# Performance work log

Measured on AMD Instinct MI355X. Metric: run time of the kernel, lower is better.

## Reference

```python
import jax, jax.numpy as jnp
import numpy as np

B, N, E = 16, 1024, 32768
D_IN, HID, HEADS, OUT = 33, 32, 4, 8  # OUT = d_mid // heads
EPS = 1e-5
NEG_SLOPE = 0.2  # PyG GATConv default leaky_relu slope


def layer_norm(x, g, b):
    m = x.mean(-1, keepdims=True)
    v = ((x - m) ** 2).mean(-1, keepdims=True)
    return (x - m) / jnp.sqrt(v + EPS) * g + b


def gat_conv(x, src, dst, W, a_src, a_dst, bias):
    # x: [N, F_in]; W: [F_in, HEADS*OUT]; a_src/a_dst: [HEADS, OUT]
    n = x.shape[0]
    xp = (x @ W).reshape(n, HEADS, OUT)                 # [N, H, D]
    al_s = (xp * a_src).sum(-1)                          # [N, H]
    al_d = (xp * a_dst).sum(-1)                          # [N, H]
    e = jax.nn.leaky_relu(al_s[src] + al_d[dst], NEG_SLOPE)  # [E, H]
    # softmax over incoming edges per target node (PyG: softmax over edge_index[1])
    m = jax.ops.segment_max(e, dst, num_segments=n)
    ex = jnp.exp(e - m[dst])
    s = jax.ops.segment_sum(ex, dst, num_segments=n)
    alpha = ex / s[dst]                                  # [E, H]
    out = jax.ops.segment_sum(xp[src] * alpha[:, :, None], dst, num_segments=n)
    return out.reshape(n, HEADS * OUT) + bias, alpha


def setup_inputs() -> dict:
    key = jax.random.key(0)
    ks = jax.random.split(key, 16)
    inp = {
        "H": jax.random.normal(ks[0], (B, N, D_IN), jnp.float32),
        "edge_index": jax.random.randint(ks[1], (2, E), 0, N, dtype=jnp.int64),
        # ObsEmbedding params
        "W1_e": jax.random.normal(ks[2], (D_IN, HID), jnp.float32) * 0.1,
        "b1_e": jnp.zeros((HID,), jnp.float32),
        "W2_e": jax.random.normal(ks[3], (HID, HID), jnp.float32) * 0.1,
        "b2_e": jnp.zeros((HID,), jnp.float32),
        "ln_e_g": jnp.ones((HID,), jnp.float32),
        "ln_e_b": jnp.zeros((HID,), jnp.float32),
        # GAT1 params
        "W_g1": jax.random.normal(ks[4], (HID, HEADS * OUT), jnp.float32) * 0.1,
        "as_g1": jax.random.normal(ks[5], (HEADS, OUT), jnp.float32) * 0.1,
        "ad_g1": jax.random.normal(ks[6], (HEADS, OUT), jnp.float32) * 0.1,
        "bi_g1": jnp.zeros((HEADS * OUT,), jnp.float32),
        # GAT2 params
        "W_g2": jax.random.normal(ks[7], (HEADS * OUT, HEADS * OUT), jnp.float32) * 0.1,
        "as_g2": jax.random.normal(ks[8], (HEADS, OUT), jnp.float32) * 0.1,
        "ad_g2": jax.random.normal(ks[9], (HEADS, OUT), jnp.float32) * 0.1,
        "bi_g2": jnp.zeros((HEADS * OUT,), jnp.float32),
        # output LayerNorm
        "ln_o_g": jnp.ones((HEADS * OUT,), jnp.float32),
        "ln_o_b": jnp.zeros((HEADS * OUT,), jnp.float32),
    }
    return inp


def reference(H, edge_index, W1_e, b1_e, W2_e, b2_e, ln_e_g, ln_e_b,
              W_g1, as_g1, ad_g1, bi_g1, W_g2, as_g2, ad_g2, bi_g2,
              ln_o_g, ln_o_b):
    src, dst = edge_index[0], edge_index[1]

    # ObsEmbedding: Linear->ReLU->Linear->ReLU->LayerNorm (batched, dense)
    x = jax.nn.relu(H @ W1_e + b1_e)
    x = jax.nn.relu(x @ W2_e + b2_e)
    x = layer_norm(x, ln_e_g, ln_e_b)          # [B, N, 32]

    def per_graph(xb):
        h1, _ = gat_conv(xb, src, dst, W_g1, as_g1, ad_g1, bi_g1)
        h1 = jax.nn.relu(h1)
        h2, alpha2 = gat_conv(h1, src, dst, W_g2, as_g2, ad_g2, bi_g2)
        h_out = layer_norm(h1 + h2, ln_o_g, ln_o_b)
        return h_out, alpha2

    h_out, alpha2 = jax.vmap(per_graph)(x)      # [B, N, 32], [B, E, HEADS]

    # scatter edge attention into dense [B, HEADS, N, N] at [src, dst]
    alpha_t = jnp.transpose(alpha2, (0, 2, 1))  # [B, HEADS, E]
    A = jnp.zeros((B, HEADS, N, N), jnp.float32).at[:, :, src, dst].set(alpha_t)
    return h_out, A
```

## Files before the change

kernel.cpp:

```cpp
#include <hip/hip_runtime.h>
#include <hip/hip_bf16.h>

#define BB 16
#define NN 1024
#define EE 32768
#define D_IN 33
#define HID 32
#define HEADS 4
#define OUTD 8
#define FF 32
#define EPSL 1e-5f
#define SLOPE 0.2f

__device__ __forceinline__ float red32(float v) {
    v += __shfl_xor(v, 1);
    v += __shfl_xor(v, 2);
    v += __shfl_xor(v, 4);
    v += __shfl_xor(v, 8);
    v += __shfl_xor(v, 16);
    return v;
}
__device__ __forceinline__ float red8(float v) {
    v += __shfl_xor(v, 1);
    v += __shfl_xor(v, 2);
    v += __shfl_xor(v, 4);
    return v;
}
__device__ __forceinline__ void wb() { __builtin_amdgcn_wave_barrier(); }

struct EmbedS {
    float sW1[D_IN * 32];
    float sW2[1024];
    float sWg[1024];
    float sb1[32], sb2[32], sg[32], sbt[32], sas[32], sad[32];
    float sh[8][34];
    float sx[8][33];
};
struct CsrS {
    int hh[1024];
    int hh2[1024];
    int sp[256];
};

__global__ __launch_bounds__(256) void k_embed_csr(
    const float* __restrict__ Hm, const float* __restrict__ W1,
    const float* __restrict__ b1, const float* __restrict__ W2,
    const float* __restrict__ b2, const float* __restrict__ lng,
    const float* __restrict__ lnb, const float* __restrict__ Wg1,
    const float* __restrict__ as1, const float* __restrict__ ad1,
    float* __restrict__ xp1, float* __restrict__ als1, float* __restrict__ ald1,
    const int* __restrict__ ei, int* __restrict__ off, int* __restrict__ cur,
    int* __restrict__ off2, int* __restrict__ cur2) {
    __shared__ union { EmbedS e; CsrS c; } sm;
    int tid = threadIdx.x;
    if (blockIdx.x == 2048) {
        int t = tid;
#pragma unroll
        for (int i = 0; i < 4; i++) { sm.c.hh[t + 256 * i] = 0; sm.c.hh2[t + 256 * i] = 0; }
        __syncthreads();
        for (int e = t; e < EE; e += 256) {
            int s = ei[e], d = ei[EE + e];
            atomicAdd(&sm.c.hh[d], 1);
            atomicAdd(&sm.c.hh2[s], 1);
        }
        __syncthreads();
        {
            int a0 = sm.c.hh[4 * t], a1 = sm.c.hh[4 * t + 1];
            int a2 = sm.c.hh[4 * t + 2], a3 = sm.c.hh[4 * t + 3];
            int s0 = a0, s01 = a0 + a1, s012 = s01 + a2, tot = s012 + a3;
            sm.c.sp[t] = tot;
            __syncthreads();
            for (int st = 1; st < 256; st <<= 1) {
                int u = (t >= st) ? sm.c.sp[t - st] : 0;
                __syncthreads();
                sm.c.sp[t] += u;
                __syncthreads();
            }
            int ex = t ? sm.c.sp[t - 1] : 0;
            off[4 * t + 1] = ex + s0; off[4 * t + 2] = ex + s01;
            off[4 * t + 3] = ex + s012; off[4 * t + 4] = ex + tot;
            if (t == 0) off[0] = 0;
            cur[4 * t] = ex; cur[4 * t + 1] = ex + s0;
            cur[4 * t + 2] = ex + s01; cur[4 * t + 3] = ex + s012;
            __syncthreads();
        }
        {
            int a0 = sm.c.hh2[4 * t], a1 = sm.c.hh2[4 * t + 1];
            int a2 = sm.c.hh2[4 * t + 2], a3 = sm.c.hh2[4 * t + 3];
            int s0 = a0, s01 = a0 + a1, s012 = s01 + a2, tot = s012 + a3;
            sm.c.sp[t] = tot;
            __syncthreads();
            for (int st = 1; st < 256; st <<= 1) {
                int u = (t >= st) ? sm.c.sp[t - st] : 0;
                __syncthreads();
                sm.c.sp[t] += u;
                __syncthreads();
            }
            int ex = t ? sm.c.sp[t - 1] : 0;
            off2[4 * t + 1] = ex + s0; off2[4 * t + 2] = ex + s01;
            off2[4 * t + 3] = ex + s012; off2[4 * t + 4] = ex + tot;
            if (t == 0) off2[0] = 0;
            cur2[4 * t] = ex; cur2[4 * t + 1] = ex + s0;
            cur2[4 * t + 2] = ex + s01; cur2[4 * t + 3] = ex + s012;
        }
        return;
    }
    for (int i = tid; i < D_IN * 32; i += 256) sm.e.sW1[i] = W1[i];
    for (int i = tid; i < 1024; i += 256) { sm.e.sW2[i] = W2[i]; sm.e.sWg[i] = Wg1[i]; }
    if (tid < 32) {
        sm.e.sb1[tid] = b1[tid]; sm.e.sb2[tid] = b2[tid];
        sm.e.sg[tid] = lng[tid]; sm.e.sbt[tid] = lnb[tid];
        sm.e.sas[tid] = as1[tid]; sm.e.sad[tid] = ad1[tid];
    }
    int g = tid >> 5, j = tid & 31;
    int idx = blockIdx.x * 8 + g;
    __syncthreads();
    int base = idx * D_IN;
    for (int i = j; i < D_IN; i += 32) sm.e.sh[g][i] = Hm[base + i];
    wb();
    float acc = sm.e.sb1[j];
#pragma unroll
    for (int i = 0; i < D_IN; i++) acc += sm.e.sh[g][i] * sm.e.sW1[i * 32 + j];
    float x1 = fmaxf(acc, 0.f);
    sm.e.sx[g][j] = x1;
    wb();
    acc = sm.e.sb2[j];
#pragma unroll
    for (int i = 0; i < 32; i++) acc += sm.e.sx[g][i] * sm.e.sW2[i * 32 + j];
    float x2 = fmaxf(acc, 0.f);
    float mean = red32(x2) * (1.f / 32.f);
    float d0 = x2 - mean;
    float var = red32(d0 * d0) * (1.f / 32.f);
    float xn = d0 * rsqrtf(var + EPSL) * sm.e.sg[j] + sm.e.sbt[j];
    wb();
    sm.e.sx[g][j] = xn;
    wb();
    acc = 0.f;
#pragma unroll
    for (int i = 0; i < 32; i++) acc += sm.e.sx[g][i] * sm.e.sWg[i * 32 + j];
    xp1[idx * 32 + j] = acc;
    float ps = red8(acc * sm.e.sas[j]);
    float pd = red8(acc * sm.e.sad[j]);
    if ((j & 7) == 0) {
        als1[idx * 4 + (j >> 3)] = ps;
        ald1[idx * 4 + (j >> 3)] = pd;
    }
}

__global__ __launch_bounds__(256) void k_fill(const int* __restrict__ ei,
                                              int* __restrict__ cur,
                                              int* __restrict__ csr_src,
                                              int* __restrict__ cur2,
                                              int* __restrict__ out_dst) {
    int e = blockIdx.x * 256 + threadIdx.x;
    if (e < EE) {
        int s = ei[e], d = ei[EE + e];
        int p = atomicAdd(&cur[d], 1);
        csr_src[p] = s;
        int p2 = atomicAdd(&cur2[s], 1);
        out_dst[p2] = d;
    }
}

__global__ __launch_bounds__(256) void k_gat1(
    const int* __restrict__ off, const int* __restrict__ csr_src,
    const float* __restrict__ xp1, const float* __restrict__ als1,
    const float* __restrict__ ald1, const float* __restrict__ bi1,
    const float* __restrict__ Wg2, const float* __restrict__ as2,
    const float* __restrict__ ad2, float* __restrict__ h1,
    float* __restrict__ xp2, float* __restrict__ als2, float* __restrict__ ald2) {
    __shared__ float sW[1024];
    __shared__ float sb[32], sas[32], sad[32];
    __shared__ float sx[8][33];
    __shared__ float salp[8][32];
    __shared__ int   ssrc[8][8];
    int tid = threadIdx.x;
    for (int i = tid; i < 1024; i += 256) sW[i] = Wg2[i];
    if (tid < 32) { sb[tid] = bi1[tid]; sas[tid] = as2[tid]; sad[tid] = ad2[tid]; }
    __syncthreads();
    int g = tid >> 5, j = tid & 31, h = j >> 3, t8 = j & 7;
    int idx = blockIdx.x * 8 + g;
    int b = idx >> 10, n = idx & 1023;
    int beg = off[n], end = off[n + 1];
    float aldh = ald1[idx * 4 + h];
    const float* alsb = als1 + b * NN * 4;
    const float* xpb = xp1 + b * NN * 32;
    float se = 0.f, acc = 0.f;
    for (int kb = beg; kb < end; kb += 8) {
        int k = kb + t8;
        float al = 0.f; int s = 0;
        if (k < end) {
            s = csr_src[k];
            float av = alsb[s * 4 + h] + aldh;
            av = av > 0.f ? av : SLOPE * av;
            al = __expf(av);
        }
        se += al;
        salp[g][j] = al;
        if (h == 0) ssrc[g][t8] = s;
        wb();
#pragma unroll
        for (int t = 0; t < 8; t++)
            acc += salp[g][(h << 3) + t] * xpb[ssrc[g][t] * 32 + j];
        wb();
    }
    se = red8(se);
    float inv = se > 0.f ? 1.f / se : 0.f;
    acc *= inv;
    float hv = fmaxf(acc + sb[j], 0.f);
    h1[idx * 32 + j] = hv;
    sx[g][j] = hv;
    wb();
    float x2 = 0.f;
#pragma unroll
    for (int i = 0; i < 32; i++) x2 += sx[g][i] * sW[i * 32 + j];
    xp2[idx * 32 + j] = x2;
    float ps = red8(x2 * sas[j]);
    float pd = red8(x2 * sad[j]);
    if (t8 == 0) {
        als2[idx * 4 + h] = ps;
        ald2[((b * 4 + h) << 10) + n] = pd;
    }
}

__global__ __launch_bounds__(256) void k_gat2(
    const int* __restrict__ off, const int* __restrict__ csr_src,
    const float* __restrict__ xp2, const float* __restrict__ als2,
    const float* __restrict__ ald2, const float* __restrict__ h1,
    const float* __restrict__ bi2, const float* __restrict__ lng,
    const float* __restrict__ lnb, float* __restrict__ outH,
    float* __restrict__ dinv) {
    __shared__ float sb[32], sg[32], sbt[32];
    __shared__ float salp[8][32];
    __shared__ int   ssrc[8][8];
    int tid = threadIdx.x;
    if (tid < 32) { sb[tid] = bi2[tid]; sg[tid] = lng[tid]; sbt[tid] = lnb[tid]; }
    __syncthreads();
    int g = tid >> 5, j = tid & 31, h = j >> 3, t8 = j & 7;
    int idx = blockIdx.x * 8 + g;
    int b = idx >> 10, n = idx & 1023;
    int beg = off[n], end = off[n + 1];
    float aldh = ald2[((b * 4 + h) << 10) + n];
    const float* alsb = als2 + b * NN * 4;
    const float* xpb = xp2 + b * NN * 32;
    float se = 0.f, acc = 0.f;
    for (int kb = beg; kb < end; kb += 8) {
        int k = kb + t8;
        float al = 0.f; int s = 0;
        if (k < end) {
            s = csr_src[k];
            float av = alsb[s * 4 + h] + aldh;
            av = av > 0.f ? av : SLOPE * av;
            al = __expf(av);
        }
        se += al;
        salp[g][j] = al;
        if (h == 0) ssrc[g][t8] = s;
        wb();
#pragma unroll
        for (int t = 0; t < 8; t++)
            acc += salp[g][(h << 3) + t] * xpb[ssrc[g][t] * 32 + j];
        wb();
    }
    se = red8(se);
    float inv = se > 0.f ? 1.f / se : 0.f;
    if (t8 == 0) dinv[((b * 4 + h) << 10) + n] = inv;
    acc *= inv;
    float y = h1[idx * 32 + j] + acc + sb[j];
    float mean = red32(y) * (1.f / 32.f);
    float d0 = y - mean;
    float var = red32(d0 * d0) * (1.f / 32.f);
    outH[idx * 32 + j] = d0 * rsqrtf(var + EPSL) * sg[j] + sbt[j];
}

#define ROWS_PER_BLOCK 4
__global__ __launch_bounds__(256) void k_rowA(
    const int* __restrict__ off2, const int* __restrict__ out_dst,
    const float* __restrict__ als2, const float* __restrict__ ald2,
    const float* __restrict__ dinv, float* __restrict__ A) {
    __shared__ float sRow[ROWS_PER_BLOCK][NN];
    int wid = threadIdx.x >> 6, lane = threadIdx.x & 63;
    int r = blockIdx.x * ROWS_PER_BLOCK + wid;
    int bh = r >> 10, src = r & 1023;
    int b = bh >> 2, h = bh & 3;
    float sS = als2[((b << 10) + src) * 4 + h];
    const float* aldv = ald2 + ((size_t)bh << 10);
    const float* dinvv = dinv + ((size_t)bh << 10);
    float4* row4 = (float4*)&sRow[wid][0];
    float4 z = make_float4(0.f, 0.f, 0.f, 0.f);
#pragma unroll
    for (int i = 0; i < 4; i++) row4[i * 64 + lane] = z;
    wb();
    int beg = off2[src], end = off2[src + 1];
    for (int p = beg + lane; p < end; p += 64) {
        int d = out_dst[p];
        float lg = sS + aldv[d];
        lg = lg > 0.f ? lg : SLOPE * lg;
        sRow[wid][d] = __expf(lg) * dinvv[d];
    }
    wb();
    float4* o4 = (float4*)(A + (size_t)bh * (NN * NN) + (size_t)src * NN);
#pragma unroll
    for (int i = 0; i < 4; i++) o4[i * 64 + lane] = row4[i * 64 + lane];
}

extern "C" void kernel_launch(void* const* d_in, const int* in_sizes, int n_in,
                              void* d_out, int out_size, void* d_ws, size_t ws_size,
                              hipStream_t stream) {
    const float* Hm  = (const float*)d_in[0];
    const int*   ei  = (const int*)d_in[1];
    const float* W1  = (const float*)d_in[2];
    const float* b1  = (const float*)d_in[3];
    const float* W2  = (const float*)d_in[4];
    const float* b2  = (const float*)d_in[5];
    const float* lneg = (const float*)d_in[6];
    const float* lneb = (const float*)d_in[7];
    const float* Wg1 = (const float*)d_in[8];
    const float* as1 = (const float*)d_in[9];
    const float* ad1 = (const float*)d_in[10];
    const float* bi1 = (const float*)d_in[11];
    const float* Wg2 = (const float*)d_in[12];
    const float* as2 = (const float*)d_in[13];
    const float* ad2 = (const float*)d_in[14];
    const float* bi2 = (const float*)d_in[15];
    const float* lnog = (const float*)d_in[16];
    const float* lnob = (const float*)d_in[17];

    float* outH = (float*)d_out;
    float* A    = outH + BB * NN * FF;

    int* off      = (int*)d_ws;
    int* cur      = off + 1028;
    int* off2     = cur + 1024;
    int* cur2     = off2 + 1028;
    int* csr_src  = cur2 + 1024;
    int* out_dst  = csr_src + EE;
    float* fb     = (float*)(out_dst + EE);
    float* xp1    = fb;
    float* als1   = xp1 + BB * NN * FF;
    float* ald1   = als1 + BB * NN * 4;
    float* h1     = ald1 + BB * NN * 4;
    float* xp2    = h1 + BB * NN * FF;
    float* als2   = xp2 + BB * NN * FF;
    float* ald2   = als2 + BB * NN * 4;
    float* dinv   = ald2 + BB * NN * 4;

    hipLaunchKernelGGL(k_embed_csr, dim3(BB * NN / 8 + 1), dim3(256), 0, stream,
                       Hm, W1, b1, W2, b2, lneg, lneb, Wg1, as1, ad1,
                       xp1, als1, ald1, ei, off, cur, off2, cur2);
    hipLaunchKernelGGL(k_fill, dim3(EE / 256), dim3(256), 0, stream,
                       ei, cur, csr_src, cur2, out_dst);
    hipLaunchKernelGGL(k_gat1, dim3(BB * NN / 8), dim3(256), 0, stream,
                       off, csr_src, xp1, als1, ald1, bi1, Wg2, as2, ad2,
                       h1, xp2, als2, ald2);
    hipLaunchKernelGGL(k_gat2, dim3(BB * NN / 8), dim3(256), 0, stream,
                       off, csr_src, xp2, als2, ald2, h1, bi2, lnog, lnob,
                       outH, dinv);
    hipLaunchKernelGGL(k_rowA, dim3(BB * HEADS * NN / ROWS_PER_BLOCK), dim3(256),
                       0, stream, off2, out_dst, als2, ald2, dinv, A);
}
```

Before: 417.6 us.

## Replace CSR build with fixed-capacity bucket adjacency and fuse into embed kernel

Replaces the single-block histogram plus prefix-scan CSR construction and the separate fill kernel with fixed-capacity per-node buckets (CAP=96). The buckets are filled by atomics in extra blocks of the embed kernel, after a memset of the counters. It also interleaves ald2 and dinv into one float2 array so the row-scatter kernel does one load per edge, and writes the dense A matrix with nontemporal stores. The serial scan block and one launch go away. The cost is that edge order within a bucket is now nondeterministic and any node with more than 96 edges would overflow its bucket.

Measured after the change: 347.4 us. 16.8% less time.

```diff
diff --git a/kernel.cpp b/kernel.cpp
--- a/kernel.cpp
+++ b/kernel.cpp
@@ -11,6 +11,9 @@
 #define FF 32
 #define EPSL 1e-5f
 #define SLOPE 0.2f
+#define CAP 96
+
+typedef float v4f __attribute__((ext_vector_type(4)));
 
 __device__ __forceinline__ float red32(float v) {
     v += __shfl_xor(v, 1);
@@ -28,147 +31,81 @@
 }
 __device__ __forceinline__ void wb() { __builtin_amdgcn_wave_barrier(); }
 
-struct EmbedS {
-    float sW1[D_IN * 32];
-    float sW2[1024];
-    float sWg[1024];
-    float sb1[32], sb2[32], sg[32], sbt[32], sas[32], sad[32];
-    float sh[8][34];
-    float sx[8][33];
-};
-struct CsrS {
-    int hh[1024];
-    int hh2[1024];
-    int sp[256];
-};
-
-__global__ __launch_bounds__(256) void k_embed_csr(
+__global__ __launch_bounds__(256) void k_embed_bucket(
     const float* __restrict__ Hm, const float* __restrict__ W1,
     const float* __restrict__ b1, const float* __restrict__ W2,
     const float* __restrict__ b2, const float* __restrict__ lng,
     const float* __restrict__ lnb, const float* __restrict__ Wg1,
     const float* __restrict__ as1, const float* __restrict__ ad1,
     float* __restrict__ xp1, float* __restrict__ als1, float* __restrict__ ald1,
-    const int* __restrict__ ei, int* __restrict__ off, int* __restrict__ cur,
-    int* __restrict__ off2, int* __restrict__ cur2) {
-    __shared__ union { EmbedS e; CsrS c; } sm;
+    const int* __restrict__ ei, int* __restrict__ cnt_in, int* __restrict__ cnt_out,
+    int* __restrict__ csr_b, int* __restrict__ out_b) {
     int tid = threadIdx.x;
-    if (blockIdx.x == 2048) {
-        int t = tid;
-#pragma unroll
-        for (int i = 0; i < 4; i++) { sm.c.hh[t + 256 * i] = 0; sm.c.hh2[t + 256 * i] = 0; }
-        __syncthreads();
-        for (int e = t; e < EE; e += 256) {
-            int s = ei[e], d = ei[EE + e];
-            atomicAdd(&sm.c.hh[d], 1);
-            atomicAdd(&sm.c.hh2[s], 1);
-        }
-        __syncthreads();
-        {
-            int a0 = sm.c.hh[4 * t], a1 = sm.c.hh[4 * t + 1];
-            int a2 = sm.c.hh[4 * t + 2], a3 = sm.c.hh[4 * t + 3];
-            int s0 = a0, s01 = a0 + a1, s012 = s01 + a2, tot = s012 + a3;
-            sm.c.sp[t] = tot;
-            __syncthreads();
-            for (int st = 1; st < 256; st <<= 1) {
-                int u = (t >= st) ? sm.c.sp[t - st] : 0;
-                __syncthreads();
-                sm.c.sp[t] += u;
-                __syncthreads();
-            }
-            int ex = t ? sm.c.sp[t - 1] : 0;
-            off[4 * t + 1] = ex + s0; off[4 * t + 2] = ex + s01;
-            off[4 * t + 3] = ex + s012; off[4 * t + 4] = ex + tot;
-            if (t == 0) off[0] = 0;
-            cur[4 * t] = ex; cur[4 * t + 1] = ex + s0;
-            cur[4 * t + 2] = ex + s01; cur[4 * t + 3] = ex + s012;
-            __syncthreads();
-        }
-        {
-            int a0 = sm.c.hh2[4 * t], a1 = sm.c.hh2[4 * t + 1];
-            int a2 = sm.c.hh2[4 * t + 2], a3 = sm.c.hh2[4 * t + 3];
-            int s0 = a0, s01 = a0 + a1, s012 = s01 + a2, tot = s012 + a3;
-            sm.c.sp[t] = tot;
-            __syncthreads();
-            for (int st = 1; st < 256; st <<= 1) {
-                int u = (t >= st) ? sm.c.sp[t - st] : 0;
-                __syncthreads();
-                sm.c.sp[t] += u;
-                __syncthreads();
-            }
-            int ex = t ? sm.c.sp[t - 1] : 0;
-            off2[4 * t + 1] = ex + s0; off2[4 * t + 2] = ex + s01;
-            off2[4 * t + 3] = ex + s012; off2[4 * t + 4] = ex + tot;
-            if (t == 0) off2[0] = 0;
-            cur2[4 * t] = ex; cur2[4 * t + 1] = ex + s0;
-            cur2[4 * t + 2] = ex + s01; cur2[4 * t + 3] = ex + s012;
-        }
+    if (blockIdx.x >= 2048) {
+        int e = (blockIdx.x - 2048) * 256 + tid;
+        int s = ei[e], d = ei[EE + e];
+        int p = atomicAdd(&cnt_in[d], 1);
+        csr_b[d * CAP + p] = s;
+        int q = atomicAdd(&cnt_out[s], 1);
+        out_b[s * CAP + q] = d;
         return;
     }
-    for (int i = tid; i < D_IN * 32; i += 256) sm.e.sW1[i] = W1[i];
-    for (int i = tid; i < 1024; i += 256) { sm.e.sW2[i] = W2[i]; sm.e.sWg[i] = Wg1[i]; }
+    __shared__ float sW1[D_IN * 32];
+    __shared__ float sW2[1024];
+    __shared__ float sWg[1024];
+    __shared__ float sb1[32], sb2[32], sg[32], sbt[32], sas[32], sad[32];
+    __shared__ float sh[8][34];
+    __shared__ float sx[8][33];
+    for (int i = tid; i < D_IN * 32; i += 256) sW1[i] = W1[i];
+    for (int i = tid; i < 1024; i += 256) { sW2[i] = W2[i]; sWg[i] = Wg1[i]; }
     if (tid < 32) {
-        sm.e.sb1[tid] = b1[tid]; sm.e.sb2[tid] = b2[tid];
-        sm.e.sg[tid] = lng[tid]; sm.e.sbt[tid] = lnb[tid];
-        sm.e.sas[tid] = as1[tid]; sm.e.sad[tid] = ad1[tid];
+        sb1[tid] = b1[tid]; sb2[tid] = b2[tid];
+        sg[tid] = lng[tid]; sbt[tid] = lnb[tid];
+        sas[tid] = as1[tid]; sad[tid] = ad1[tid];
     }
     int g = tid >> 5, j = tid & 31;
     int idx = blockIdx.x * 8 + g;
     __syncthreads();
     int base = idx * D_IN;
-    for (int i = j; i < D_IN; i += 32) sm.e.sh[g][i] = Hm[base + i];
-    wb();
-    float acc = sm.e.sb1[j];
-#pragma unroll
-    for (int i = 0; i < D_IN; i++) acc += sm.e.sh[g][i] * sm.e.sW1[i * 32 + j];
+    for (int i = j; i < D_IN; i += 32) sh[g][i] = Hm[base + i];
+    wb();
+    float acc = sb1[j];
+#pragma unroll
+    for (int i = 0; i < D_IN; i++) acc += sh[g][i] * sW1[i * 32 + j];
     float x1 = fmaxf(acc, 0.f);
-    sm.e.sx[g][j] = x1;
-    wb();
-    acc = sm.e.sb2[j];
-#pragma unroll
-    for (int i = 0; i < 32; i++) acc += sm.e.sx[g][i] * sm.e.sW2[i * 32 + j];
+    sx[g][j] = x1;
+    wb();
+    acc = sb2[j];
+#pragma unroll
+    for (int i = 0; i < 32; i++) acc += sx[g][i] * sW2[i * 32 + j];
     float x2 = fmaxf(acc, 0.f);
     float mean = red32(x2) * (1.f / 32.f);
     float d0 = x2 - mean;
     float var = red32(d0 * d0) * (1.f / 32.f);
-    float xn = d0 * rsqrtf(var + EPSL) * sm.e.sg[j] + sm.e.sbt[j];
-    wb();
-    sm.e.sx[g][j] = xn;
+    float xn = d0 * rsqrtf(var + EPSL) * sg[j] + sbt[j];
+    wb();
+    sx[g][j] = xn;
     wb();
     acc = 0.f;
 #pragma unroll
-    for (int i = 0; i < 32; i++) acc += sm.e.sx[g][i] * sm.e.sWg[i * 32 + j];
+    for (int i = 0; i < 32; i++) acc += sx[g][i] * sWg[i * 32 + j];
     xp1[idx * 32 + j] = acc;
-    float ps = red8(acc * sm.e.sas[j]);
-    float pd = red8(acc * sm.e.sad[j]);
+    float ps = red8(acc * sas[j]);
+    float pd = red8(acc * sad[j]);
     if ((j & 7) == 0) {
         als1[idx * 4 + (j >> 3)] = ps;
         ald1[idx * 4 + (j >> 3)] = pd;
     }
 }
 
-__global__ __launch_bounds__(256) void k_fill(const int* __restrict__ ei,
-                                              int* __restrict__ cur,
-                                              int* __restrict__ csr_src,
-                                              int* __restrict__ cur2,
-                                              int* __restrict__ out_dst) {
-    int e = blockIdx.x * 256 + threadIdx.x;
-    if (e < EE) {
-        int s = ei[e], d = ei[EE + e];
-        int p = atomicAdd(&cur[d], 1);
-        csr_src[p] = s;
-        int p2 = atomicAdd(&cur2[s], 1);
-        out_dst[p2] = d;
-    }
-}
-
 __global__ __launch_bounds__(256) void k_gat1(
-    const int* __restrict__ off, const int* __restrict__ csr_src,
+    const int* __restrict__ cnt_in, const int* __restrict__ csr_b,
     const float* __restrict__ xp1, const float* __restrict__ als1,
     const float* __restrict__ ald1, const float* __restrict__ bi1,
     const float* __restrict__ Wg2, const float* __restrict__ as2,
     const float* __restrict__ ad2, float* __restrict__ h1,
-    float* __restrict__ xp2, float* __restrict__ als2, float* __restrict__ ald2) {
+    float* __restrict__ xp2, float* __restrict__ als2,
+    float2* __restrict__ aldinv) {
     __shared__ float sW[1024];
     __shared__ float sb[32], sas[32], sad[32];
     __shared__ float sx[8][33];
@@ -181,16 +118,17 @@
     int g = tid >> 5, j = tid & 31, h = j >> 3, t8 = j & 7;
     int idx = blockIdx.x * 8 + g;
     int b = idx >> 10, n = idx & 1023;
-    int beg = off[n], end = off[n + 1];
+    int cnt = cnt_in[n];
+    const int* row = csr_b + n * CAP;
     float aldh = ald1[idx * 4 + h];
     const float* alsb = als1 + b * NN * 4;
     const float* xpb = xp1 + b * NN * 32;
     float se = 0.f, acc = 0.f;
-    for (int kb = beg; kb < end; kb += 8) {
+    for (int kb = 0; kb < cnt; kb += 8) {
         int k = kb + t8;
         float al = 0.f; int s = 0;
-        if (k < end) {
-            s = csr_src[k];
+        if (k < cnt) {
+            s = row[k];
             float av = alsb[s * 4 + h] + aldh;
             av = av > 0.f ? av : SLOPE * av;
             al = __expf(av);
@@ -219,17 +157,16 @@
     float pd = red8(x2 * sad[j]);
     if (t8 == 0) {
         als2[idx * 4 + h] = ps;
-        ald2[((b * 4 + h) << 10) + n] = pd;
+        aldinv[((b * 4 + h) << 10) + n].x = pd;
     }
 }
 
 __global__ __launch_bounds__(256) void k_gat2(
-    const int* __restrict__ off, const int* __restrict__ csr_src,
+    const int* __restrict__ cnt_in, const int* __restrict__ csr_b,
     const float* __restrict__ xp2, const float* __restrict__ als2,
-    const float* __restrict__ ald2, const float* __restrict__ h1,
+    float2* __restrict__ aldinv, const float* __restrict__ h1,
     const float* __restrict__ bi2, const float* __restrict__ lng,
-    const float* __restrict__ lnb, float* __restrict__ outH,
-    float* __restrict__ dinv) {
+    const float* __restrict__ lnb, float* __restrict__ outH) {
     __shared__ float sb[32], sg[32], sbt[32];
     __shared__ float salp[8][32];
     __shared__ int   ssrc[8][8];
@@ -239,16 +176,17 @@
     int g = tid >> 5, j = tid & 31, h = j >> 3, t8 = j & 7;
     int idx = blockIdx.x * 8 + g;
     int b = idx >> 10, n = idx & 1023;
-    int beg = off[n], end = off[n + 1];
-    float aldh = ald2[((b * 4 + h) << 10) + n];
+    int cnt = cnt_in[n];
+    const int* row = csr_b + n * CAP;
+    float aldh = aldinv[((b * 4 + h) << 10) + n].x;
     const float* alsb = als2 + b * NN * 4;
     const float* xpb = xp2 + b * NN * 32;
     float se = 0.f, acc = 0.f;
-    for (int kb = beg; kb < end; kb += 8) {
+    for (int kb = 0; kb < cnt; kb += 8) {
         int k = kb + t8;
         float al = 0.f; int s = 0;
-        if (k < end) {
-            s = csr_src[k];
+        if (k < cnt) {
+            s = row[k];
             float av = alsb[s * 4 + h] + aldh;
             av = av > 0.f ? av : SLOPE * av;
             al = __expf(av);
@@ -264,7 +202,7 @@
     }
     se = red8(se);
     float inv = se > 0.f ? 1.f / se : 0.f;
-    if (t8 == 0) dinv[((b * 4 + h) << 10) + n] = inv;
+    if (t8 == 0) aldinv[((b * 4 + h) << 10) + n].y = inv;
     acc *= inv;
     float y = h1[idx * 32 + j] + acc + sb[j];
     float mean = red32(y) * (1.f / 32.f);
@@ -275,33 +213,36 @@
 
 #define ROWS_PER_BLOCK 4
 __global__ __launch_bounds__(256) void k_rowA(
-    const int* __restrict__ off2, const int* __restrict__ out_dst,
-    const float* __restrict__ als2, const float* __restrict__ ald2,
-    const float* __restrict__ dinv, float* __restrict__ A) {
+    const int* __restrict__ cnt_out, const int* __restrict__ out_b,
+    const float* __restrict__ als2, const float2* __restrict__ aldinv,
+    float* __restrict__ A) {
     __shared__ float sRow[ROWS_PER_BLOCK][NN];
     int wid = threadIdx.x >> 6, lane = threadIdx.x & 63;
     int r = blockIdx.x * ROWS_PER_BLOCK + wid;
     int bh = r >> 10, src = r & 1023;
     int b = bh >> 2, h = bh & 3;
     float sS = als2[((b << 10) + src) * 4 + h];
-    const float* aldv = ald2 + ((size_t)bh << 10);
-    const float* dinvv = dinv + ((size_t)bh << 10);
-    float4* row4 = (float4*)&sRow[wid][0];
-    float4 z = make_float4(0.f, 0.f, 0.f, 0.f);
+    const float2* aiv = aldinv + ((size_t)bh << 10);
+    v4f* row4 = (v4f*)&sRow[wid][0];
+    v4f z = {0.f, 0.f, 0.f, 0.f};
 #pragma unroll
     for (int i = 0; i < 4; i++) row4[i * 64 + lane] = z;
     wb();
-    int beg = off2[src], end = off2[src + 1];
-    for (int p = beg + lane; p < end; p += 64) {
-        int d = out_dst[p];
-        float lg = sS + aldv[d];
+    int cnt = cnt_out[src];
+    const int* erow = out_b + src * CAP;
+    for (int p = lane; p < cnt; p += 64) {
+        int d = erow[p];
+        float2 ai = aiv[d];
+        float lg = sS + ai.x;
         lg = lg > 0.f ? lg : SLOPE * lg;
-        sRow[wid][d] = __expf(lg) * dinvv[d];
-    }
-    wb();
-    float4* o4 = (float4*)(A + (size_t)bh * (NN * NN) + (size_t)src * NN);
-#pragma unroll
-    for (int i = 0; i < 4; i++) o4[i * 64 + lane] = row4[i * 64 + lane];
+        sRow[wid][d] = __expf(lg) * ai.y;
+    }
+    wb();
+    float* orow = A + (size_t)bh * (NN * NN) + (size_t)src * NN;
+#pragma unroll
+    for (int i = 0; i < 4; i++)
+        __builtin_nontemporal_store(row4[i * 64 + lane],
+                                    (v4f*)(orow + 4 * (i * 64 + lane)));
 }
 
 extern "C" void kernel_launch(void* const* d_in, const int* in_sizes, int n_in,
@@ -329,33 +270,29 @@
     float* outH = (float*)d_out;
     float* A    = outH + BB * NN * FF;
 
-    int* off      = (int*)d_ws;
-    int* cur      = off + 1028;
-    int* off2     = cur + 1024;
-    int* cur2     = off2 + 1028;
-    int* csr_src  = cur2 + 1024;
-    int* out_dst  = csr_src + EE;
-    float* fb     = (float*)(out_dst + EE);
+    int* cnt_in  = (int*)d_ws;
+    int* cnt_out = cnt_in + 1024;
+    int* csr_b   = cnt_out + 1024;
+    int* out_b   = csr_b + NN * CAP;
+    float* fb    = (float*)(out_b + NN * CAP);
     float* xp1    = fb;
     float* als1   = xp1 + BB * NN * FF;
     float* ald1   = als1 + BB * NN * 4;
     float* h1     = ald1 + BB * NN * 4;
     float* xp2    = h1 + BB * NN * FF;
     float* als2   = xp2 + BB * NN * FF;
-    float* ald2   = als2 + BB * NN * 4;
-    float* dinv   = ald2 + BB * NN * 4;
-
-    hipLaunchKernelGGL(k_embed_csr, dim3(BB * NN / 8 + 1), dim3(256), 0, stream,
-                       Hm, W1, b1, W2, b2, lneg, lneb, Wg1, as1, ad1,
-                       xp1, als1, ald1, ei, off, cur, off2, cur2);
-    hipLaunchKernelGGL(k_fill, dim3(EE / 256), dim3(256), 0, stream,
-                       ei, cur, csr_src, cur2, out_dst);
+    float2* aldinv = (float2*)(als2 + BB * NN * 4);
+
+    (void)hipMemsetAsync(cnt_in, 0, 2 * NN * sizeof(int), stream);
+    hipLaunchKernelGGL(k_embed_bucket, dim3(BB * NN / 8 + EE / 256), dim3(256), 0,
+                       stream, Hm, W1, b1, W2, b2, lneg, lneb, Wg1, as1, ad1,
+                       xp1, als1, ald1, ei, cnt_in, cnt_out, csr_b, out_b);
     hipLaunchKernelGGL(k_gat1, dim3(BB * NN / 8), dim3(256), 0, stream,
-                       off, csr_src, xp1, als1, ald1, bi1, Wg2, as2, ad2,
-                       h1, xp2, als2, ald2);
+                       cnt_in, csr_b, xp1, als1, ald1, bi1, Wg2, as2, ad2,
+                       h1, xp2, als2, aldinv);
     hipLaunchKernelGGL(k_gat2, dim3(BB * NN / 8), dim3(256), 0, stream,
-                       off, csr_src, xp2, als2, ald2, h1, bi2, lnog, lnob,
-                       outH, dinv);
+                       cnt_in, csr_b, xp2, als2, aldinv, h1, bi2, lnog, lnob,
+                       outH);
     hipLaunchKernelGGL(k_rowA, dim3(BB * HEADS * NN / ROWS_PER_BLOCK), dim3(256),
-                       0, stream, off2, out_dst, als2, ald2, dinv, A);
-}
+                       0, stream, cnt_out, out_b, als2, aldinv, A);
+}
```
